# Kernel tuning notes

Hardware: AMD Instinct MI355X
Metric: run time of the kernel (lower is better)

Reference implementation:

```python
import jax, jax.numpy as jnp
import numpy as np

# Forest of B complete binary trees: L leaves, NPT = 2L-1 nodes per tree.
B, L, H = 128, 512, 128
NPT = 2 * L - 1
N = B * NPT
VOCAB, OUT = 32000, 128


def _levels():
    """Static topo schedule: per internal level, (node, left_child, right_child) global ids."""
    tree_off = np.arange(B, dtype=np.int32)[:, None] * NPT  # [B,1]
    levels = []
    off, cnt = 0, L
    while cnt > 1:
        child_off = off
        off += cnt
        cnt //= 2
        node = off + np.arange(cnt, dtype=np.int32)
        left = child_off + 2 * np.arange(cnt, dtype=np.int32)
        right = left + 1
        levels.append(tuple(jnp.asarray((a[None, :] + tree_off).ravel())
                            for a in (node, left, right)))
    roots = jnp.asarray((tree_off[:, 0] + (NPT - 1)).astype(np.int32))
    leaves = jnp.asarray((np.arange(L, dtype=np.int32)[None, :] + tree_off).ravel())
    return levels, roots, leaves


def setup_inputs() -> dict:
    key = jax.random.key(0)
    ks = jax.random.split(key, 8)
    s = lambda k, shp, sc: jax.random.normal(k, shp, jnp.float32) * sc
    return {
        "label": jax.random.randint(ks[0], (N,), 0, VOCAB),
        "emb": s(ks[1], (VOCAB, H), 0.02),
        "W_iou": s(ks[2], (H, 3 * H), H ** -0.5),
        "U_iou": s(ks[3], (2 * H, 3 * H), (2 * H) ** -0.5),
        "b_iou": jnp.zeros((3 * H,), jnp.float32),
        "U_f_w": s(ks[4], (2 * H, 2 * H), (2 * H) ** -0.5),
        "U_f_b": jnp.zeros((2 * H,), jnp.float32),
        "W_out": s(ks[5], (H, OUT), H ** -0.5),
        "b_out": jnp.zeros((OUT,), jnp.float32),
    }


def _apply_node(iou, b_iou, c_in):
    # apply_node_func: gates + LSTM cell update
    i, o, u = jnp.split(iou + b_iou, 3, axis=-1)
    c = jax.nn.sigmoid(i) * jnp.tanh(u) + c_in
    h = jax.nn.sigmoid(o) * jnp.tanh(c)
    return h, c


def reference(label, emb, W_iou, U_iou, b_iou, U_f_w, U_f_b, W_out, b_out):
    levels, roots, leaves = _levels()
    iou0 = emb[label] @ W_iou                      # [N, 3H] W_iou(emb(label)) for every node
    h = jnp.zeros((N, H), iou0.dtype)
    c = jnp.zeros((N, H), iou0.dtype)
    # leaves: no incoming messages, c_in = 0
    hl, cl = _apply_node(iou0[leaves], b_iou, 0.0)
    h = h.at[leaves].set(hl)
    c = c.at[leaves].set(cl)
    # internal frontiers in topological order (fan-in = 2)
    for node, left, right in levels:
        h_cat = jnp.concatenate([h[left], h[right]], axis=-1)   # [n_d, 2H]
        f = jax.nn.sigmoid(h_cat @ U_f_w + U_f_b)               # forget gates per child
        fl, fr = jnp.split(f, 2, axis=-1)
        c_red = fl * c[left] + fr * c[right]                    # child-sum of gated cells
        iou = h_cat @ U_iou                                     # reduce_func overwrites iou
        hn, cn = _apply_node(iou, b_iou, c_red)
        h = h.at[node].set(hn)
        c = c.at[node].set(cn)
    final = h[roots] @ W_out + b_out                            # root hidden per tree
    return jax.nn.log_softmax(final, axis=-1)
```

## Files before the change

### kernel.cpp

```cpp
#include <hip/hip_runtime.h>
#include <math.h>

#define B_    128
#define L_    512
#define H_    128
#define NPT_  1023
#define N_    (B_ * NPT_)
#define NLEAF (B_ * L_)
#define OUT_  128
#define VOCAB 32000
#define TBASE 992

typedef unsigned short ushort_t;
typedef __attribute__((ext_vector_type(8))) __bf16 bf16x8;
typedef __attribute__((ext_vector_type(4))) float f32x4;

__device__ __forceinline__ float sigmoidf_(float x) {
    return 1.0f / (1.0f + __expf(-x));
}
__device__ __forceinline__ float tanhf_(float x) {
    return 1.0f - 2.0f / (__expf(2.0f * x) + 1.0f);
}
__device__ __forceinline__ ushort_t f2bf(float f) {
    unsigned u = __float_as_uint(f);
    return (ushort_t)((u + 0x7fffu + ((u >> 16) & 1u)) >> 16);
}
__device__ __forceinline__ float bf2f(ushort_t s) {
    return __uint_as_float(((unsigned)s) << 16);
}

__global__ __launch_bounds__(256)
void prep_fused(const float* __restrict__ W_iou,
                const float* __restrict__ U_iou,
                const float* __restrict__ U_f_w,
                const float* __restrict__ emb,
                ushort_t* __restrict__ W_iouT,
                ushort_t* __restrict__ U_catT,
                ushort_t* __restrict__ embb) {
    int idx = blockIdx.x * 256 + threadIdx.x;
    if (idx < VOCAB * H_ / 8) {
        int e0 = idx * 8;
        f32x4 f0 = *(const f32x4*)(emb + e0);
        f32x4 f1 = *(const f32x4*)(emb + e0 + 4);
        union { bf16x8 v; ushort_t e[8]; } p;
        p.e[0] = f2bf(f0[0]); p.e[1] = f2bf(f0[1]);
        p.e[2] = f2bf(f0[2]); p.e[3] = f2bf(f0[3]);
        p.e[4] = f2bf(f1[0]); p.e[5] = f2bf(f1[1]);
        p.e[6] = f2bf(f1[2]); p.e[7] = f2bf(f1[3]);
        *(bf16x8*)(embb + e0) = p.v;
    }
    if (idx < 640 * 256) {
        int n = idx >> 8, k = idx & 255;
        float v = (n < 384) ? U_iou[k * 384 + n] : U_f_w[k * 256 + (n - 384)];
        U_catT[idx] = f2bf(v);
    }
    if (idx < 384 * 128) {
        int n = idx >> 7, k = idx & 127;
        W_iouT[idx] = f2bf(W_iou[k * 384 + n]);
    }
}

__global__ __launch_bounds__(256, 4)
void leaf_v3(const int* __restrict__ label,
             const ushort_t* __restrict__ embb,
             const ushort_t* __restrict__ WT,
             const float* __restrict__ b_iou,
             ushort_t* __restrict__ h,
             float* __restrict__ c,
             int ntiles, int stripes) {
    const int tid  = threadIdx.x;
    const int lane = tid & 63;
    const int wave = tid >> 6;
    const int li   = lane & 15;
    const int q    = lane >> 4;
    const int q8   = q << 3;
    const int gg   = blockIdx.y * 4 + wave;
    const int j    = gg * 16 + li;

    bf16x8 Bf[3][4];
    #pragma unroll
    for (int t = 0; t < 3; ++t) {
        const ushort_t* bp = WT + (size_t)(16 * (gg + 8 * t) + li) * 128 + q8;
        #pragma unroll
        for (int kt = 0; kt < 4; ++kt) Bf[t][kt] = *(const bf16x8*)(bp + kt * 32);
    }

    const float bi = b_iou[j], bo = b_iou[128 + j], bu = b_iou[256 + j];

    for (int tile = blockIdx.x; tile < ntiles; tile += stripes) {
        const int i0 = tile * 16;
        int ia = i0 + li, ba = ia >> 9, pa = ia & 511;
        const ushort_t* pA = embb + (size_t)label[ba * NPT_ + pa] * H_;
        bf16x8 a[4];
        #pragma unroll
        for (int kt = 0; kt < 4; ++kt) a[kt] = *(const bf16x8*)(pA + kt * 32 + q8);

        f32x4 acc[3];
        #pragma unroll
        for (int t = 0; t < 3; ++t) acc[t] = (f32x4){0.f, 0.f, 0.f, 0.f};
        #pragma unroll
        for (int kt = 0; kt < 4; ++kt)
            #pragma unroll
            for (int t = 0; t < 3; ++t)
                acc[t] = __builtin_amdgcn_mfma_f32_16x16x32_bf16(a[kt], Bf[t][kt], acc[t], 0, 0, 0);

        #pragma unroll
        for (int r = 0; r < 4; ++r) {
            int m  = i0 + q * 4 + r;
            int b  = m >> 9, pos = m & 511;
            size_t gn = (size_t)(b * NPT_ + pos) * H_ + j;
            float iv = sigmoidf_(acc[0][r] + bi);
            float ov = sigmoidf_(acc[1][r] + bo);
            float uv = tanhf_(acc[2][r] + bu);
            float cv = iv * uv;
            float hv = ov * tanhf_(cv);
            c[gn] = cv;
            h[gn] = f2bf(hv);
        }
    }
}

__global__ __launch_bounds__(256, 2)
void level_v3(const ushort_t* __restrict__ Ucat,
              const float* __restrict__ b_iou,
              const float* __restrict__ U_f_b,
              ushort_t* __restrict__ h,
              float* __restrict__ c,
              int node_base, int child_base, int lc,
              int ntiles, int stripes) {
    const int tid  = threadIdx.x;
    const int lane = tid & 63;
    const int wave = tid >> 6;
    const int li   = lane & 15;
    const int q    = lane >> 4;
    const int q8   = q << 3;
    const int mask = (1 << lc) - 1;
    const int gg   = blockIdx.y * 4 + wave;
    const int j    = gg * 16 + li;

    bf16x8 Bf[5][8];
    #pragma unroll
    for (int t = 0; t < 5; ++t) {
        const ushort_t* bp = Ucat + (size_t)(16 * (gg + 8 * t) + li) * 256 + q8;
        #pragma unroll
        for (int kt = 0; kt < 8; ++kt) Bf[t][kt] = *(const bf16x8*)(bp + kt * 32);
    }

    const float bi  = b_iou[j], bo = b_iou[128 + j], bu = b_iou[256 + j];
    const float bfl = U_f_b[j], bfr = U_f_b[128 + j];

    for (int tile = blockIdx.x; tile < ntiles; tile += stripes) {
        const int i0 = tile * 16;
        float clv[4], crv[4];
        int   gnrow[4];
        #pragma unroll
        for (int r = 0; r < 4; ++r) {
            int m = i0 + q * 4 + r;
            int b = m >> lc, pos = m & mask;
            int gl = b * NPT_ + child_base + 2 * pos;
            gnrow[r] = b * NPT_ + node_base + pos;
            clv[r] = c[(size_t)gl * H_ + j];
            crv[r] = c[(size_t)(gl + 1) * H_ + j];
        }
        int ia = i0 + li, ba = ia >> lc, pa = ia & mask;
        int gl0 = ba * NPT_ + child_base + 2 * pa;
        const ushort_t* pl = h + (size_t)gl0 * H_;
        const ushort_t* pr = h + (size_t)(gl0 + 1) * H_;
        bf16x8 a[8];
        #pragma unroll
        for (int kt = 0; kt < 8; ++kt) {
            const ushort_t* p = (kt < 4) ? pl : pr;
            a[kt] = *(const bf16x8*)(p + (kt & 3) * 32 + q8);
        }
        f32x4 acc[5];
        #pragma unroll
        for (int t = 0; t < 5; ++t) acc[t] = (f32x4){0.f, 0.f, 0.f, 0.f};
        #pragma unroll
        for (int kt = 0; kt < 8; ++kt)
            #pragma unroll
            for (int t = 0; t < 5; ++t)
                acc[t] = __builtin_amdgcn_mfma_f32_16x16x32_bf16(a[kt], Bf[t][kt], acc[t], 0, 0, 0);
        #pragma unroll
        for (int r = 0; r < 4; ++r) {
            size_t gn = (size_t)gnrow[r] * H_ + j;
            float iv = sigmoidf_(acc[0][r] + bi);
            float ov = sigmoidf_(acc[1][r] + bo);
            float uv = tanhf_(acc[2][r] + bu);
            float fl = sigmoidf_(acc[3][r] + bfl);
            float fr = sigmoidf_(acc[4][r] + bfr);
            float cv = iv * uv + fl * clv[r] + fr * crv[r];
            float hv = ov * tanhf_(cv);
            c[gn] = cv;
            h[gn] = f2bf(hv);
        }
    }
}

#define TPAD 132
__global__ __launch_bounds__(512, 2)
void tail_kernel(const ushort_t* __restrict__ Ucat,
                 const float* __restrict__ b_iou,
                 const float* __restrict__ U_f_b,
                 const ushort_t* __restrict__ h,
                 const float* __restrict__ c,
                 const float* __restrict__ W_out,
                 const float* __restrict__ b_out,
                 float* __restrict__ out) {
    __shared__ ushort_t hl[31][TPAD];
    __shared__ float    cl[31][TPAD];
    __shared__ float    ev[H_];
    __shared__ float    red[128];

    const int tid  = threadIdx.x;
    const int lane = tid & 63;
    const int wave = tid >> 6;
    const int li   = lane & 15;
    const int q    = lane >> 4;
    const int q8   = q << 3;
    const int gg   = wave;
    const int j    = gg * 16 + li;
    const int b    = blockIdx.x;

    bf16x8 Bf[5][8];
    #pragma unroll
    for (int t = 0; t < 5; ++t) {
        const ushort_t* bp = Ucat + (size_t)(16 * (gg + 8 * t) + li) * 256 + q8;
        #pragma unroll
        for (int kt = 0; kt < 8; ++kt) Bf[t][kt] = *(const bf16x8*)(bp + kt * 32);
    }

    const float bi  = b_iou[j], bo = b_iou[128 + j], bu = b_iou[256 + j];
    const float bfl = U_f_b[j], bfr = U_f_b[128 + j];

    int base = TBASE, child = 960, cnt = 16;
    #pragma unroll
    for (int lvl = 0; lvl < 5; ++lvl) {
        int pos = li < cnt ? li : cnt - 1;
        bf16x8 a[8];
        if (lvl == 0) {
            int gl0 = b * NPT_ + child + 2 * pos;
            const ushort_t* pl = h + (size_t)gl0 * H_;
            const ushort_t* pr = h + (size_t)(gl0 + 1) * H_;
            #pragma unroll
            for (int kt = 0; kt < 8; ++kt) {
                const ushort_t* p = (kt < 4) ? pl : pr;
                a[kt] = *(const bf16x8*)(p + (kt & 3) * 32 + q8);
            }
        } else {
            int tl = (child - TBASE) + 2 * pos;
            #pragma unroll
            for (int kt = 0; kt < 8; ++kt) {
                const ushort_t* p = (kt < 4) ? hl[tl] : hl[tl + 1];
                a[kt] = *(const bf16x8*)(p + (kt & 3) * 32 + q8);
            }
        }

        float clv[4], crv[4];
        #pragma unroll
        for (int r = 0; r < 4; ++r) {
            int m  = q * 4 + r;
            int pm = m < cnt ? m : cnt - 1;
            if (lvl == 0) {
                int gl = b * NPT_ + child + 2 * pm;
                clv[r] = c[(size_t)gl * H_ + j];
                crv[r] = c[(size_t)(gl + 1) * H_ + j];
            } else {
                int tl = (child - TBASE) + 2 * pm;
                clv[r] = cl[tl][j];
                crv[r] = cl[tl + 1][j];
            }
        }

        f32x4 acc[5];
        #pragma unroll
        for (int t = 0; t < 5; ++t) acc[t] = (f32x4){0.f, 0.f, 0.f, 0.f};
        #pragma unroll
        for (int kt = 0; kt < 8; ++kt)
            #pragma unroll
            for (int t = 0; t < 5; ++t)
                acc[t] = __builtin_amdgcn_mfma_f32_16x16x32_bf16(a[kt], Bf[t][kt], acc[t], 0, 0, 0);

        #pragma unroll
        for (int r = 0; r < 4; ++r) {
            int m = q * 4 + r;
            if (m < cnt) {
                int tl = (base - TBASE) + m;
                float iv = sigmoidf_(acc[0][r] + bi);
                float ov = sigmoidf_(acc[1][r] + bo);
                float uv = tanhf_(acc[2][r] + bu);
                float fl = sigmoidf_(acc[3][r] + bfl);
                float fr = sigmoidf_(acc[4][r] + bfr);
                float cv = iv * uv + fl * clv[r] + fr * crv[r];
                float hv = ov * tanhf_(cv);
                cl[tl][j] = cv;
                hl[tl][j] = f2bf(hv);
            }
        }
        __syncthreads();
        child = base; base += cnt; cnt >>= 1;
    }

    if (tid < 128) ev[tid] = bf2f(hl[30][tid]);
    __syncthreads();

    float acc = 0.0f;
    if (tid < 128) {
        acc = b_out[tid];
        for (int k = 0; k < H_; ++k)
            acc += ev[k] * W_out[k * OUT_ + tid];
        red[tid] = acc;
    }
    __syncthreads();
    for (int s = 64; s > 0; s >>= 1) {
        if (tid < s) red[tid] = fmaxf(red[tid], red[tid + s]);
        __syncthreads();
    }
    float mx = red[0];
    __syncthreads();
    if (tid < 128) red[tid] = expf(acc - mx);
    __syncthreads();
    for (int s = 64; s > 0; s >>= 1) {
        if (tid < s) red[tid] += red[tid + s];
        __syncthreads();
    }
    float lse = logf(red[0]);
    if (tid < 128) out[b * OUT_ + tid] = acc - mx - lse;
}

extern "C" void kernel_launch(void* const* d_in, const int* in_sizes, int n_in,
                              void* d_out, int out_size, void* d_ws, size_t ws_size,
                              hipStream_t stream) {
    const int*   label = (const int*)d_in[0];
    const float* emb   = (const float*)d_in[1];
    const float* W_iou = (const float*)d_in[2];
    const float* U_iou = (const float*)d_in[3];
    const float* b_iou = (const float*)d_in[4];
    const float* U_f_w = (const float*)d_in[5];
    const float* U_f_b = (const float*)d_in[6];
    const float* W_out = (const float*)d_in[7];
    const float* b_out = (const float*)d_in[8];
    float* outp = (float*)d_out;

    float*    c    = (float*)d_ws;
    ushort_t* h    = (ushort_t*)(c + (size_t)N_ * H_);
    ushort_t* Ucat = h + (size_t)N_ * H_;
    ushort_t* WT   = Ucat + 640 * 256;
    ushort_t* embb = WT + 384 * 128;

    prep_fused<<<2000, 256, 0, stream>>>(W_iou, U_iou, U_f_w, emb, WT, Ucat, embb);

    {
        int ntiles = NLEAF / 16, stripes = 512;
        leaf_v3<<<dim3(stripes, 2), 256, 0, stream>>>(
            label, embb, WT, b_iou, h, c, ntiles, stripes);
    }

    int child = 0, node = 512, cnt = 256, lc = 8;
    for (int lvl = 0; lvl < 4; ++lvl) {
        int ntiles  = (B_ * cnt) / 16;
        int stripes = ntiles < 256 ? ntiles : 256;
        level_v3<<<dim3(stripes, 2), 256, 0, stream>>>(
            Ucat, b_iou, U_f_b, h, c, node, child, lc, ntiles, stripes);
        child = node; node += cnt; cnt >>= 1; --lc;
    }

    tail_kernel<<<B_, 512, 0, stream>>>(Ucat, b_iou, U_f_b, h, c, W_out, b_out, outp);
}
```

Before: 221.9 us.

## Widen level tiles to 32 rows, fold one more level into tail, prefetch leaf labels

The level kernel now processes two 16-row sub-tiles per iteration, so each loaded weight fragment feeds twice as many MFMAs and more child-state loads are in flight. The last global level launch is removed and its work moves into the per-tree tail kernel, which now handles six levels in LDS starting from 32 nodes. The leaf kernel preloads all eight label indices up front and drops the generic stripe loop. The cost is more registers in the level kernel, about twice the LDS in the tail, and more serial work for each tail block.

```diff
diff --git a/kernel.cpp b/kernel.cpp
--- a/kernel.cpp
+++ b/kernel.cpp
@@ -9,7 +9,7 @@
 #define NLEAF (B_ * L_)
 #define OUT_  128
 #define VOCAB 32000
-#define TBASE 992
+#define TBASE 960
 
 typedef unsigned short ushort_t;
 typedef __attribute__((ext_vector_type(8))) __bf16 bf16x8;
@@ -66,8 +66,7 @@
              const ushort_t* __restrict__ WT,
              const float* __restrict__ b_iou,
              ushort_t* __restrict__ h,
-             float* __restrict__ c,
-             int ntiles, int stripes) {
+             float* __restrict__ c) {
     const int tid  = threadIdx.x;
     const int lane = tid & 63;
     const int wave = tid >> 6;
@@ -85,12 +84,21 @@
         for (int kt = 0; kt < 4; ++kt) Bf[t][kt] = *(const bf16x8*)(bp + kt * 32);
     }
 
+    int lab[8];
+    #pragma unroll
+    for (int t = 0; t < 8; ++t) {
+        int ia = (blockIdx.x + t * 512) * 16 + li;
+        int ba = ia >> 9, pa = ia & 511;
+        lab[t] = label[ba * NPT_ + pa];
+    }
+
     const float bi = b_iou[j], bo = b_iou[128 + j], bu = b_iou[256 + j];
 
-    for (int tile = blockIdx.x; tile < ntiles; tile += stripes) {
+    #pragma unroll 1
+    for (int t8 = 0; t8 < 8; ++t8) {
+        const int tile = blockIdx.x + t8 * 512;
         const int i0 = tile * 16;
-        int ia = i0 + li, ba = ia >> 9, pa = ia & 511;
-        const ushort_t* pA = embb + (size_t)label[ba * NPT_ + pa] * H_;
+        const ushort_t* pA = embb + (size_t)lab[t8] * H_;
         bf16x8 a[4];
         #pragma unroll
         for (int kt = 0; kt < 4; ++kt) a[kt] = *(const bf16x8*)(pA + kt * 32 + q8);
@@ -121,13 +129,13 @@
 }
 
 __global__ __launch_bounds__(256, 2)
-void level_v3(const ushort_t* __restrict__ Ucat,
-              const float* __restrict__ b_iou,
-              const float* __restrict__ U_f_b,
-              ushort_t* __restrict__ h,
-              float* __restrict__ c,
-              int node_base, int child_base, int lc,
-              int ntiles, int stripes) {
+void level_v32(const ushort_t* __restrict__ Ucat,
+               const float* __restrict__ b_iou,
+               const float* __restrict__ U_f_b,
+               ushort_t* __restrict__ h,
+               float* __restrict__ c,
+               int node_base, int child_base, int lc,
+               int ntiles, int stripes) {
     const int tid  = threadIdx.x;
     const int lane = tid & 63;
     const int wave = tid >> 6;
@@ -149,49 +157,67 @@
     const float bi  = b_iou[j], bo = b_iou[128 + j], bu = b_iou[256 + j];
     const float bfl = U_f_b[j], bfr = U_f_b[128 + j];
 
+    #pragma unroll 1
     for (int tile = blockIdx.x; tile < ntiles; tile += stripes) {
-        const int i0 = tile * 16;
-        float clv[4], crv[4];
-        int   gnrow[4];
-        #pragma unroll
-        for (int r = 0; r < 4; ++r) {
-            int m = i0 + q * 4 + r;
-            int b = m >> lc, pos = m & mask;
-            int gl = b * NPT_ + child_base + 2 * pos;
-            gnrow[r] = b * NPT_ + node_base + pos;
-            clv[r] = c[(size_t)gl * H_ + j];
-            crv[r] = c[(size_t)(gl + 1) * H_ + j];
-        }
-        int ia = i0 + li, ba = ia >> lc, pa = ia & mask;
-        int gl0 = ba * NPT_ + child_base + 2 * pa;
-        const ushort_t* pl = h + (size_t)gl0 * H_;
-        const ushort_t* pr = h + (size_t)(gl0 + 1) * H_;
-        bf16x8 a[8];
+        const int i0 = tile * 32;
+
+        float clv[2][4], crv[2][4];
+        int   gnrow[2][4];
+        #pragma unroll
+        for (int sub = 0; sub < 2; ++sub) {
+            #pragma unroll
+            for (int r = 0; r < 4; ++r) {
+                int m = i0 + sub * 16 + q * 4 + r;
+                int b = m >> lc, pos = m & mask;
+                int gl = b * NPT_ + child_base + 2 * pos;
+                gnrow[sub][r] = b * NPT_ + node_base + pos;
+                clv[sub][r] = c[(size_t)gl * H_ + j];
+                crv[sub][r] = c[(size_t)(gl + 1) * H_ + j];
+            }
+        }
+
+        const ushort_t *pl[2], *pr[2];
+        #pragma unroll
+        for (int sub = 0; sub < 2; ++sub) {
+            int ia = i0 + sub * 16 + li, ba = ia >> lc, pa = ia & mask;
+            int gl0 = ba * NPT_ + child_base + 2 * pa;
+            pl[sub] = h + (size_t)gl0 * H_;
+            pr[sub] = h + (size_t)(gl0 + 1) * H_;
+        }
+
+        f32x4 acc[2][5];
+        #pragma unroll
+        for (int s = 0; s < 2; ++s)
+            #pragma unroll
+            for (int t = 0; t < 5; ++t) acc[s][t] = (f32x4){0.f, 0.f, 0.f, 0.f};
+
         #pragma unroll
         for (int kt = 0; kt < 8; ++kt) {
-            const ushort_t* p = (kt < 4) ? pl : pr;
-            a[kt] = *(const bf16x8*)(p + (kt & 3) * 32 + q8);
-        }
-        f32x4 acc[5];
-        #pragma unroll
-        for (int t = 0; t < 5; ++t) acc[t] = (f32x4){0.f, 0.f, 0.f, 0.f};
-        #pragma unroll
-        for (int kt = 0; kt < 8; ++kt)
-            #pragma unroll
-            for (int t = 0; t < 5; ++t)
-                acc[t] = __builtin_amdgcn_mfma_f32_16x16x32_bf16(a[kt], Bf[t][kt], acc[t], 0, 0, 0);
-        #pragma unroll
-        for (int r = 0; r < 4; ++r) {
-            size_t gn = (size_t)gnrow[r] * H_ + j;
-            float iv = sigmoidf_(acc[0][r] + bi);
-            float ov = sigmoidf_(acc[1][r] + bo);
-            float uv = tanhf_(acc[2][r] + bu);
-            float fl = sigmoidf_(acc[3][r] + bfl);
-            float fr = sigmoidf_(acc[4][r] + bfr);
-            float cv = iv * uv + fl * clv[r] + fr * crv[r];
-            float hv = ov * tanhf_(cv);
-            c[gn] = cv;
-            h[gn] = f2bf(hv);
+            const int ko = (kt & 3) * 32 + q8;
+            bf16x8 a0 = *(const bf16x8*)(((kt < 4) ? pl[0] : pr[0]) + ko);
+            bf16x8 a1 = *(const bf16x8*)(((kt < 4) ? pl[1] : pr[1]) + ko);
+            #pragma unroll
+            for (int t = 0; t < 5; ++t) {
+                acc[0][t] = __builtin_amdgcn_mfma_f32_16x16x32_bf16(a0, Bf[t][kt], acc[0][t], 0, 0, 0);
+                acc[1][t] = __builtin_amdgcn_mfma_f32_16x16x32_bf16(a1, Bf[t][kt], acc[1][t], 0, 0, 0);
+            }
+        }
+
+        #pragma unroll
+        for (int sub = 0; sub < 2; ++sub) {
+            #pragma unroll
+            for (int r = 0; r < 4; ++r) {
+                size_t gn = (size_t)gnrow[sub][r] * H_ + j;
+                float iv = sigmoidf_(acc[sub][0][r] + bi);
+                float ov = sigmoidf_(acc[sub][1][r] + bo);
+                float uv = tanhf_(acc[sub][2][r] + bu);
+                float fl = sigmoidf_(acc[sub][3][r] + bfl);
+                float fr = sigmoidf_(acc[sub][4][r] + bfr);
+                float cv = iv * uv + fl * clv[sub][r] + fr * crv[sub][r];
+                float hv = ov * tanhf_(cv);
+                c[gn] = cv;
+                h[gn] = f2bf(hv);
+            }
         }
     }
 }
@@ -206,8 +232,8 @@
                  const float* __restrict__ W_out,
                  const float* __restrict__ b_out,
                  float* __restrict__ out) {
-    __shared__ ushort_t hl[31][TPAD];
-    __shared__ float    cl[31][TPAD];
+    __shared__ ushort_t hl[63][TPAD];
+    __shared__ float    cl[63][TPAD];
     __shared__ float    ev[H_];
     __shared__ float    red[128];
 
@@ -232,75 +258,80 @@
     const float bi  = b_iou[j], bo = b_iou[128 + j], bu = b_iou[256 + j];
     const float bfl = U_f_b[j], bfr = U_f_b[128 + j];
 
-    int base = TBASE, child = 960, cnt = 16;
-    #pragma unroll
-    for (int lvl = 0; lvl < 5; ++lvl) {
-        int pos = li < cnt ? li : cnt - 1;
-        bf16x8 a[8];
-        if (lvl == 0) {
-            int gl0 = b * NPT_ + child + 2 * pos;
-            const ushort_t* pl = h + (size_t)gl0 * H_;
-            const ushort_t* pr = h + (size_t)(gl0 + 1) * H_;
-            #pragma unroll
-            for (int kt = 0; kt < 8; ++kt) {
-                const ushort_t* p = (kt < 4) ? pl : pr;
-                a[kt] = *(const bf16x8*)(p + (kt & 3) * 32 + q8);
-            }
-        } else {
-            int tl = (child - TBASE) + 2 * pos;
-            #pragma unroll
-            for (int kt = 0; kt < 8; ++kt) {
-                const ushort_t* p = (kt < 4) ? hl[tl] : hl[tl + 1];
-                a[kt] = *(const bf16x8*)(p + (kt & 3) * 32 + q8);
-            }
-        }
-
-        float clv[4], crv[4];
-        #pragma unroll
-        for (int r = 0; r < 4; ++r) {
-            int m  = q * 4 + r;
-            int pm = m < cnt ? m : cnt - 1;
+    int base = TBASE, child = 896, cnt = 32;
+    #pragma unroll 1
+    for (int lvl = 0; lvl < 6; ++lvl) {
+        const int tiles = (cnt + 15) >> 4;
+        for (int tile = 0; tile < tiles; ++tile) {
+            const int i0 = tile * 16;
+
+            int pos = i0 + li; if (pos >= cnt) pos = cnt - 1;
+            bf16x8 a[8];
             if (lvl == 0) {
-                int gl = b * NPT_ + child + 2 * pm;
-                clv[r] = c[(size_t)gl * H_ + j];
-                crv[r] = c[(size_t)(gl + 1) * H_ + j];
+                int gl0 = b * NPT_ + child + 2 * pos;
+                const ushort_t* pl = h + (size_t)gl0 * H_;
+                const ushort_t* pr = h + (size_t)(gl0 + 1) * H_;
+                #pragma unroll
+                for (int kt = 0; kt < 8; ++kt) {
+                    const ushort_t* p = (kt < 4) ? pl : pr;
+                    a[kt] = *(const bf16x8*)(p + (kt & 3) * 32 + q8);
+                }
             } else {
-                int tl = (child - TBASE) + 2 * pm;
-                clv[r] = cl[tl][j];
-                crv[r] = cl[tl + 1][j];
-            }
-        }
-
-        f32x4 acc[5];
-        #pragma unroll
-        for (int t = 0; t < 5; ++t) acc[t] = (f32x4){0.f, 0.f, 0.f, 0.f};
-        #pragma unroll
-        for (int kt = 0; kt < 8; ++kt)
-            #pragma unroll
-            for (int t = 0; t < 5; ++t)
-                acc[t] = __builtin_amdgcn_mfma_f32_16x16x32_bf16(a[kt], Bf[t][kt], acc[t], 0, 0, 0);
-
-        #pragma unroll
-        for (int r = 0; r < 4; ++r) {
-            int m = q * 4 + r;
-            if (m < cnt) {
-                int tl = (base - TBASE) + m;
-                float iv = sigmoidf_(acc[0][r] + bi);
-                float ov = sigmoidf_(acc[1][r] + bo);
-                float uv = tanhf_(acc[2][r] + bu);
-                float fl = sigmoidf_(acc[3][r] + bfl);
-                float fr = sigmoidf_(acc[4][r] + bfr);
-                float cv = iv * uv + fl * clv[r] + fr * crv[r];
-                float hv = ov * tanhf_(cv);
-                cl[tl][j] = cv;
-                hl[tl][j] = f2bf(hv);
+                int tl = (child - TBASE) + 2 * pos;
+                #pragma unroll
+                for (int kt = 0; kt < 8; ++kt) {
+                    const ushort_t* p = (kt < 4) ? hl[tl] : hl[tl + 1];
+                    a[kt] = *(const bf16x8*)(p + (kt & 3) * 32 + q8);
+                }
+            }
+
+            float clv[4], crv[4];
+            #pragma unroll
+            for (int r = 0; r < 4; ++r) {
+                int m  = i0 + q * 4 + r;
+                int pm = m < cnt ? m : cnt - 1;
+                if (lvl == 0) {
+                    int gl = b * NPT_ + child + 2 * pm;
+                    clv[r] = c[(size_t)gl * H_ + j];
+                    crv[r] = c[(size_t)(gl + 1) * H_ + j];
+                } else {
+                    int tl = (child - TBASE) + 2 * pm;
+                    clv[r] = cl[tl][j];
+                    crv[r] = cl[tl + 1][j];
+                }
+            }
+
+            f32x4 acc[5];
+            #pragma unroll
+            for (int t = 0; t < 5; ++t) acc[t] = (f32x4){0.f, 0.f, 0.f, 0.f};
+            #pragma unroll
+            for (int kt = 0; kt < 8; ++kt)
+                #pragma unroll
+                for (int t = 0; t < 5; ++t)
+                    acc[t] = __builtin_amdgcn_mfma_f32_16x16x32_bf16(a[kt], Bf[t][kt], acc[t], 0, 0, 0);
+
+            #pragma unroll
+            for (int r = 0; r < 4; ++r) {
+                int m = i0 + q * 4 + r;
+                if (m < cnt) {
+                    int tl = (base - TBASE) + m;
+                    float iv = sigmoidf_(acc[0][r] + bi);
+                    float ov = sigmoidf_(acc[1][r] + bo);
+                    float uv = tanhf_(acc[2][r] + bu);
+                    float fl = sigmoidf_(acc[3][r] + bfl);
+                    float fr = sigmoidf_(acc[4][r] + bfr);
+                    float cv = iv * uv + fl * clv[r] + fr * crv[r];
+                    float hv = ov * tanhf_(cv);
+                    cl[tl][j] = cv;
+                    hl[tl][j] = f2bf(hv);
+                }
             }
         }
         __syncthreads();
         child = base; base += cnt; cnt >>= 1;
     }
 
-    if (tid < 128) ev[tid] = bf2f(hl[30][tid]);
+    if (tid < 128) ev[tid] = bf2f(hl[62][tid]);
     __syncthreads();
 
     float acc = 0.0f;
@@ -349,17 +380,13 @@
 
     prep_fused<<<2000, 256, 0, stream>>>(W_iou, U_iou, U_f_w, emb, WT, Ucat, embb);
 
-    {
-        int ntiles = NLEAF / 16, stripes = 512;
-        leaf_v3<<<dim3(stripes, 2), 256, 0, stream>>>(
-            label, embb, WT, b_iou, h, c, ntiles, stripes);
-    }
+    leaf_v3<<<dim3(512, 2), 256, 0, stream>>>(label, embb, WT, b_iou, h, c);
 
     int child = 0, node = 512, cnt = 256, lc = 8;
-    for (int lvl = 0; lvl < 4; ++lvl) {
-        int ntiles  = (B_ * cnt) / 16;
+    for (int lvl = 0; lvl < 3; ++lvl) {
+        int ntiles  = (B_ * cnt) / 32;
         int stripes = ntiles < 256 ? ntiles : 256;
-        level_v3<<<dim3(stripes, 2), 256, 0, stream>>>(
+        level_v32<<<dim3(stripes, 2), 256, 0, stream>>>(
             Ucat, b_iou, U_f_b, h, c, node, child, lc, ntiles, stripes);
         child = node; node += cnt; cnt >>= 1; --lc;
     }
```

New measurement: 227.1 us. +2.3%, slower.

## Stage level weights in LDS, prefetch leaf labels, fold one more level into tail

Applied to the files above, without the earlier changes.

The per-level kernel now copies one 16-column gate slice of the concatenated U weights into shared memory per block. Each of the four waves then processes its own row tile, reading B fragments from LDS instead of holding the full set in registers, and the grid uses 8 column groups. This is meant to cut register pressure and raise occupancy, at the cost of LDS traffic inside the MFMA loop. The leaf kernel preloads all eight labels for its tiles up front, and the tail kernel now handles six levels with looped tiles, which removes one level launch.

```diff
diff --git a/kernel.cpp b/kernel.cpp
--- a/kernel.cpp
+++ b/kernel.cpp
@@ -9,7 +9,8 @@
 #define NLEAF (B_ * L_)
 #define OUT_  128
 #define VOCAB 32000
-#define TBASE 992
+#define TBASE 960
+#define BROW  264
 
 typedef unsigned short ushort_t;
 typedef __attribute__((ext_vector_type(8))) __bf16 bf16x8;
@@ -66,8 +67,7 @@
              const ushort_t* __restrict__ WT,
              const float* __restrict__ b_iou,
              ushort_t* __restrict__ h,
-             float* __restrict__ c,
-             int ntiles, int stripes) {
+             float* __restrict__ c) {
     const int tid  = threadIdx.x;
     const int lane = tid & 63;
     const int wave = tid >> 6;
@@ -85,12 +85,21 @@
         for (int kt = 0; kt < 4; ++kt) Bf[t][kt] = *(const bf16x8*)(bp + kt * 32);
     }
 
+    int lab[8];
+    #pragma unroll
+    for (int t = 0; t < 8; ++t) {
+        int ia = (blockIdx.x + t * 512) * 16 + li;
+        int ba = ia >> 9, pa = ia & 511;
+        lab[t] = label[ba * NPT_ + pa];
+    }
+
     const float bi = b_iou[j], bo = b_iou[128 + j], bu = b_iou[256 + j];
 
-    for (int tile = blockIdx.x; tile < ntiles; tile += stripes) {
+    #pragma unroll 1
+    for (int t8 = 0; t8 < 8; ++t8) {
+        const int tile = blockIdx.x + t8 * 512;
         const int i0 = tile * 16;
-        int ia = i0 + li, ba = ia >> 9, pa = ia & 511;
-        const ushort_t* pA = embb + (size_t)label[ba * NPT_ + pa] * H_;
+        const ushort_t* pA = embb + (size_t)lab[t8] * H_;
         bf16x8 a[4];
         #pragma unroll
         for (int kt = 0; kt < 4; ++kt) a[kt] = *(const bf16x8*)(pA + kt * 32 + q8);
@@ -121,13 +130,13 @@
 }
 
 __global__ __launch_bounds__(256, 2)
-void level_v3(const ushort_t* __restrict__ Ucat,
-              const float* __restrict__ b_iou,
-              const float* __restrict__ U_f_b,
-              ushort_t* __restrict__ h,
-              float* __restrict__ c,
-              int node_base, int child_base, int lc,
-              int ntiles, int stripes) {
+void level_lds(const ushort_t* __restrict__ Ucat,
+               const float* __restrict__ b_iou,
+               const float* __restrict__ U_f_b,
+               ushort_t* __restrict__ h,
+               float* __restrict__ c,
+               int node_base, int child_base, int lc, int ntiles) {
+    __shared__ ushort_t Bs[5 * 16 * BROW];
     const int tid  = threadIdx.x;
     const int lane = tid & 63;
     const int wave = tid >> 6;
@@ -135,22 +144,29 @@
     const int q    = lane >> 4;
     const int q8   = q << 3;
     const int mask = (1 << lc) - 1;
-    const int gg   = blockIdx.y * 4 + wave;
+    const int gg   = blockIdx.y;
     const int j    = gg * 16 + li;
 
-    bf16x8 Bf[5][8];
     #pragma unroll
-    for (int t = 0; t < 5; ++t) {
-        const ushort_t* bp = Ucat + (size_t)(16 * (gg + 8 * t) + li) * 256 + q8;
-        #pragma unroll
-        for (int kt = 0; kt < 8; ++kt) Bf[t][kt] = *(const bf16x8*)(bp + kt * 32);
-    }
+    for (int it = 0; it < 5; ++it) {
+        int chunk = tid + it * 256;
+        int row = chunk >> 4, seg = chunk & 15;
+        int t = row >> 4, lr = row & 15;
+        const ushort_t* src = Ucat + (size_t)(16 * (gg + 8 * t) + lr) * 256 + seg * 16;
+        ushort_t*       dst = Bs + (t * 16 + lr) * BROW + seg * 16;
+        *(f32x4*)(dst)     = *(const f32x4*)(src);
+        *(f32x4*)(dst + 8) = *(const f32x4*)(src + 8);
+    }
+    __syncthreads();
 
     const float bi  = b_iou[j], bo = b_iou[128 + j], bu = b_iou[256 + j];
     const float bfl = U_f_b[j], bfr = U_f_b[128 + j];
-
-    for (int tile = blockIdx.x; tile < ntiles; tile += stripes) {
+    const int wstride = gridDim.x * 4;
+
+    #pragma unroll 1
+    for (int tile = blockIdx.x * 4 + wave; tile < ntiles; tile += wstride) {
         const int i0 = tile * 16;
+
         float clv[4], crv[4];
         int   gnrow[4];
         #pragma unroll
@@ -162,6 +178,7 @@
             clv[r] = c[(size_t)gl * H_ + j];
             crv[r] = c[(size_t)(gl + 1) * H_ + j];
         }
+
         int ia = i0 + li, ba = ia >> lc, pa = ia & mask;
         int gl0 = ba * NPT_ + child_base + 2 * pa;
         const ushort_t* pl = h + (size_t)gl0 * H_;
@@ -172,14 +189,19 @@
             const ushort_t* p = (kt < 4) ? pl : pr;
             a[kt] = *(const bf16x8*)(p + (kt & 3) * 32 + q8);
         }
+
         f32x4 acc[5];
         #pragma unroll
         for (int t = 0; t < 5; ++t) acc[t] = (f32x4){0.f, 0.f, 0.f, 0.f};
         #pragma unroll
-        for (int kt = 0; kt < 8; ++kt)
-            #pragma unroll
-            for (int t = 0; t < 5; ++t)
-                acc[t] = __builtin_amdgcn_mfma_f32_16x16x32_bf16(a[kt], Bf[t][kt], acc[t], 0, 0, 0);
+        for (int kt = 0; kt < 8; ++kt) {
+            #pragma unroll
+            for (int t = 0; t < 5; ++t) {
+                bf16x8 bf = *(const bf16x8*)(Bs + (t * 16 + li) * BROW + kt * 32 + q8);
+                acc[t] = __builtin_amdgcn_mfma_f32_16x16x32_bf16(a[kt], bf, acc[t], 0, 0, 0);
+            }
+        }
+
         #pragma unroll
         for (int r = 0; r < 4; ++r) {
             size_t gn = (size_t)gnrow[r] * H_ + j;
@@ -206,8 +228,8 @@
                  const float* __restrict__ W_out,
                  const float* __restrict__ b_out,
                  float* __restrict__ out) {
-    __shared__ ushort_t hl[31][TPAD];
-    __shared__ float    cl[31][TPAD];
+    __shared__ ushort_t hl[63][TPAD];
+    __shared__ float    cl[63][TPAD];
     __shared__ float    ev[H_];
     __shared__ float    red[128];
 
@@ -232,75 +254,80 @@
     const float bi  = b_iou[j], bo = b_iou[128 + j], bu = b_iou[256 + j];
     const float bfl = U_f_b[j], bfr = U_f_b[128 + j];
 
-    int base = TBASE, child = 960, cnt = 16;
-    #pragma unroll
-    for (int lvl = 0; lvl < 5; ++lvl) {
-        int pos = li < cnt ? li : cnt - 1;
-        bf16x8 a[8];
-        if (lvl == 0) {
-            int gl0 = b * NPT_ + child + 2 * pos;
-            const ushort_t* pl = h + (size_t)gl0 * H_;
-            const ushort_t* pr = h + (size_t)(gl0 + 1) * H_;
-            #pragma unroll
-            for (int kt = 0; kt < 8; ++kt) {
-                const ushort_t* p = (kt < 4) ? pl : pr;
-                a[kt] = *(const bf16x8*)(p + (kt & 3) * 32 + q8);
+    int base = TBASE, child = 896, cnt = 32;
+    #pragma unroll 1
+    for (int lvl = 0; lvl < 6; ++lvl) {
+        const int tiles = (cnt + 15) >> 4;
+        for (int tile = 0; tile < tiles; ++tile) {
+            const int i0 = tile * 16;
+
+            int pos = i0 + li; if (pos >= cnt) pos = cnt - 1;
+            bf16x8 a[8];
+            if (lvl == 0) {
+                int gl0 = b * NPT_ + child + 2 * pos;
+                const ushort_t* pl = h + (size_t)gl0 * H_;
+                const ushort_t* pr = h + (size_t)(gl0 + 1) * H_;
+                #pragma unroll
+                for (int kt = 0; kt < 8; ++kt) {
+                    const ushort_t* p = (kt < 4) ? pl : pr;
+                    a[kt] = *(const bf16x8*)(p + (kt & 3) * 32 + q8);
+                }
+            } else {
+                int tl = (child - TBASE) + 2 * pos;
+                #pragma unroll
+                for (int kt = 0; kt < 8; ++kt) {
+                    const ushort_t* p = (kt < 4) ? hl[tl] : hl[tl + 1];
+                    a[kt] = *(const bf16x8*)(p + (kt & 3) * 32 + q8);
+                }
             }
-        } else {
-            int tl = (child - TBASE) + 2 * pos;
-            #pragma unroll
-            for (int kt = 0; kt < 8; ++kt) {
-                const ushort_t* p = (kt < 4) ? hl[tl] : hl[tl + 1];
-                a[kt] = *(const bf16x8*)(p + (kt & 3) * 32 + q8);
+
+            float clv[4], crv[4];
+            #pragma unroll
+            for (int r = 0; r < 4; ++r) {
+                int m  = i0 + q * 4 + r;
+                int pm = m < cnt ? m : cnt - 1;
+                if (lvl == 0) {
+                    int gl = b * NPT_ + child + 2 * pm;
+                    clv[r] = c[(size_t)gl * H_ + j];
+                    crv[r] = c[(size_t)(gl + 1) * H_ + j];
+                } else {
+                    int tl = (child - TBASE) + 2 * pm;
+                    clv[r] = cl[tl][j];
+                    crv[r] = cl[tl + 1][j];
+                }
             }
-        }
-
-        float clv[4], crv[4];
-        #pragma unroll
-        for (int r = 0; r < 4; ++r) {
-            int m  = q * 4 + r;
-            int pm = m < cnt ? m : cnt - 1;
-            if (lvl == 0) {
-                int gl = b * NPT_ + child + 2 * pm;
-                clv[r] = c[(size_t)gl * H_ + j];
-                crv[r] = c[(size_t)(gl + 1) * H_ + j];
-            } else {
-                int tl = (child - TBASE) + 2 * pm;
-                clv[r] = cl[tl][j];
-                crv[r] = cl[tl + 1][j];
-            }
-        }
-
-        f32x4 acc[5];
-        #pragma unroll
-        for (int t = 0; t < 5; ++t) acc[t] = (f32x4){0.f, 0.f, 0.f, 0.f};
-        #pragma unroll
-        for (int kt = 0; kt < 8; ++kt)
-            #pragma unroll
-            for (int t = 0; t < 5; ++t)
-                acc[t] = __builtin_amdgcn_mfma_f32_16x16x32_bf16(a[kt], Bf[t][kt], acc[t], 0, 0, 0);
-
-        #pragma unroll
-        for (int r = 0; r < 4; ++r) {
-            int m = q * 4 + r;
-            if (m < cnt) {
-                int tl = (base - TBASE) + m;
-                float iv = sigmoidf_(acc[0][r] + bi);
-                float ov = sigmoidf_(acc[1][r] + bo);
-                float uv = tanhf_(acc[2][r] + bu);
-                float fl = sigmoidf_(acc[3][r] + bfl);
-                float fr = sigmoidf_(acc[4][r] + bfr);
-                float cv = iv * uv + fl * clv[r] + fr * crv[r];
-                float hv = ov * tanhf_(cv);
-                cl[tl][j] = cv;
-                hl[tl][j] = f2bf(hv);
+
+            f32x4 acc[5];
+            #pragma unroll
+            for (int t = 0; t < 5; ++t) acc[t] = (f32x4){0.f, 0.f, 0.f, 0.f};
+            #pragma unroll
+            for (int kt = 0; kt < 8; ++kt)
+                #pragma unroll
+                for (int t = 0; t < 5; ++t)
+                    acc[t] = __builtin_amdgcn_mfma_f32_16x16x32_bf16(a[kt], Bf[t][kt], acc[t], 0, 0, 0);
+
+            #pragma unroll
+            for (int r = 0; r < 4; ++r) {
+                int m = i0 + q * 4 + r;
+                if (m < cnt) {
+                    int tl = (base - TBASE) + m;
+                    float iv = sigmoidf_(acc[0][r] + bi);
+                    float ov = sigmoidf_(acc[1][r] + bo);
+                    float uv = tanhf_(acc[2][r] + bu);
+                    float fl = sigmoidf_(acc[3][r] + bfl);
+                    float fr = sigmoidf_(acc[4][r] + bfr);
+                    float cv = iv * uv + fl * clv[r] + fr * crv[r];
+                    float hv = ov * tanhf_(cv);
+                    cl[tl][j] = cv;
+                    hl[tl][j] = f2bf(hv);
+                }
             }
         }
         __syncthreads();
         child = base; base += cnt; cnt >>= 1;
     }
 
-    if (tid < 128) ev[tid] = bf2f(hl[30][tid]);
+    if (tid < 128) ev[tid] = bf2f(hl[62][tid]);
     __syncthreads();
 
     float acc = 0.0f;
@@ -349,18 +376,14 @@
 
     prep_fused<<<2000, 256, 0, stream>>>(W_iou, U_iou, U_f_w, emb, WT, Ucat, embb);
 
-    {
-        int ntiles = NLEAF / 16, stripes = 512;
-        leaf_v3<<<dim3(stripes, 2), 256, 0, stream>>>(
-            label, embb, WT, b_iou, h, c, ntiles, stripes);
-    }
+    leaf_v3<<<dim3(512, 2), 256, 0, stream>>>(label, embb, WT, b_iou, h, c);
 
     int child = 0, node = 512, cnt = 256, lc = 8;
-    for (int lvl = 0; lvl < 4; ++lvl) {
+    for (int lvl = 0; lvl < 3; ++lvl) {
         int ntiles  = (B_ * cnt) / 16;
-        int stripes = ntiles < 256 ? ntiles : 256;
-        level_v3<<<dim3(stripes, 2), 256, 0, stream>>>(
-            Ucat, b_iou, U_f_b, h, c, node, child, lc, ntiles, stripes);
+        int stripes = ntiles / 16;
+        level_lds<<<dim3(stripes, 8), 256, 0, stream>>>(
+            Ucat, b_iou, U_f_b, h, c, node, child, lc, ntiles);
         child = node; node += cnt; cnt >>= 1; --lc;
     }
 
```

New measurement: 200.5 us, median of 2. 9.6% less time.
